# Kernel optimization log

Measured on AMD Instinct MI355X. Metric: run time of the kernel, lower is better.

Reference implementation:

```python
import jax, jax.numpy as jnp
import numpy as np

B, L_VLM, L_EXP = 4, 768, 64
L_TOT = L_VLM + L_EXP
D_VLM, D_EXP = 2048, 1024
H, DH = 8, 256
ROPE_BASE = 10000.0
SCALE = 1.0 / np.sqrt(DH).astype(np.float32)


def setup_inputs() -> dict:
    key = jax.random.key(0)
    ks = jax.random.split(key, 12)
    s = 0.02  # weight init scale
    return {
        "vlm_hidden": jax.random.normal(ks[0], (B, L_VLM, D_VLM), jnp.float32),
        "exp_hidden": jax.random.normal(ks[1], (B, L_EXP, D_EXP), jnp.float32),
        "attention_mask": jnp.zeros((B, 1, L_TOT, L_TOT), jnp.float32),  # additive mask
        "position_ids": jnp.broadcast_to(jnp.arange(L_TOT, dtype=jnp.int32)[None, :], (B, L_TOT)),
        "wq_v": jax.random.normal(ks[2], (D_VLM, H * DH), jnp.float32) * s,
        "wk_v": jax.random.normal(ks[3], (D_VLM, H * DH), jnp.float32) * s,
        "wv_v": jax.random.normal(ks[4], (D_VLM, H * DH), jnp.float32) * s,
        "wo_v": jax.random.normal(ks[5], (H * DH, D_VLM), jnp.float32) * s,
        "wq_e": jax.random.normal(ks[6], (D_EXP, H * DH), jnp.float32) * s,
        "wk_e": jax.random.normal(ks[7], (D_EXP, H * DH), jnp.float32) * s,
        "wv_e": jax.random.normal(ks[8], (D_EXP, H * DH), jnp.float32) * s,
        "wo_e": jax.random.normal(ks[9], (H * DH, D_EXP), jnp.float32) * s,
    }


def _proj(hs, w):
    # [B, L, D] @ [D, H*DH] -> [B, H, L, DH]
    b, l, _ = hs.shape
    return jnp.einsum('bld,de->ble', hs, w).reshape(b, l, H, DH).transpose(0, 2, 1, 3)


def _rope(x, cos, sin):
    # NeoX-style rotate-half (Gemma / vLLM RotaryEmbedding with rotary_dim == head_dim)
    d2 = x.shape[-1] // 2
    x1, x2 = x[..., :d2], x[..., d2:]
    return jnp.concatenate([x1 * cos - x2 * sin, x2 * cos + x1 * sin], axis=-1)


def reference(vlm_hidden, exp_hidden, attention_mask, position_ids,
              wq_v, wk_v, wv_v, wo_v, wq_e, wk_e, wv_e, wo_e):
    # 1) separate per-stream Q/K/V projections, 2) concat along sequence dim
    q = jnp.concatenate([_proj(vlm_hidden, wq_v), _proj(exp_hidden, wq_e)], axis=2)
    k = jnp.concatenate([_proj(vlm_hidden, wk_v), _proj(exp_hidden, wk_e)], axis=2)
    v = jnp.concatenate([_proj(vlm_hidden, wv_v), _proj(exp_hidden, wv_e)], axis=2)

    # 3) rotary positional embedding on the joint sequence
    inv_freq = 1.0 / (ROPE_BASE ** (jnp.arange(0, DH, 2, dtype=jnp.float32) / DH))  # [DH/2]
    freqs = position_ids.astype(jnp.float32)[:, :, None] * inv_freq                 # [B, L, DH/2]
    cos = jnp.cos(freqs)[:, None]  # [B, 1, L, DH/2]
    sin = jnp.sin(freqs)[:, None]
    q = _rope(q, cos, sin)
    k = _rope(k, cos, sin)

    # 4) masked attention over the joint sequence
    scores = jnp.einsum('bhqd,bhkd->bhqk', q, k) * SCALE + attention_mask
    probs = jax.nn.softmax(scores, axis=-1)
    out = jnp.einsum('bhqk,bhkd->bhqd', probs, v)              # [B, H, L, DH]
    out = out.transpose(0, 2, 1, 3).reshape(B, L_TOT, H * DH)  # [B, L, H*DH]

    # 5) split back and apply per-stream output projections
    vlm_out = jnp.einsum('ble,ed->bld', out[:, :L_VLM], wo_v)
    exp_out = jnp.einsum('ble,ed->bld', out[:, L_VLM:], wo_e)
    return vlm_out, exp_out
```

## Files before the change

### kernel.cpp

```cpp
#include <hip/hip_runtime.h>

typedef unsigned short u16;
using bf16x8 = __attribute__((ext_vector_type(8))) __bf16;
using f32x4  = __attribute__((ext_vector_type(4))) float;

__device__ __forceinline__ u16 f2bf(float f) {
  unsigned u = __builtin_bit_cast(unsigned, f);
  u += 0x7FFFu + ((u >> 16) & 1u);
  return (u16)(u >> 16);
}
__device__ __forceinline__ float bf2f(u16 s) {
  unsigned u = ((unsigned)s) << 16;
  return __builtin_bit_cast(float, u);
}
__device__ __forceinline__ void lds16(const void* g, void* l) {
  __builtin_amdgcn_global_load_lds(
      (const __attribute__((address_space(1))) void*)g,
      (__attribute__((address_space(3))) void*)l, 16, 0, 0);
}

#define MM(A, B, C) __builtin_amdgcn_mfma_f32_16x16x32_bf16(A, B, C, 0, 0, 0)

#define MFMA16() \
  __builtin_amdgcn_s_setprio(1); \
  acc[0][0]=MM(a0,b0,acc[0][0]); acc[0][1]=MM(a0,b1,acc[0][1]); \
  acc[0][2]=MM(a0,b2,acc[0][2]); acc[0][3]=MM(a0,b3,acc[0][3]); \
  acc[1][0]=MM(a1,b0,acc[1][0]); acc[1][1]=MM(a1,b1,acc[1][1]); \
  acc[1][2]=MM(a1,b2,acc[1][2]); acc[1][3]=MM(a1,b3,acc[1][3]); \
  acc[2][0]=MM(a2,b0,acc[2][0]); acc[2][1]=MM(a2,b1,acc[2][1]); \
  acc[2][2]=MM(a2,b2,acc[2][2]); acc[2][3]=MM(a2,b3,acc[2][3]); \
  acc[3][0]=MM(a3,b0,acc[3][0]); acc[3][1]=MM(a3,b1,acc[3][1]); \
  acc[3][2]=MM(a3,b2,acc[3][2]); acc[3][3]=MM(a3,b3,acc[3][3]); \
  __builtin_amdgcn_s_setprio(0);

__device__ __forceinline__ void gemm_rg(
    const u16* aS0, const u16* aS1, const u16* bS0,
    int NT, int t, u16* As, u16* Bs, f32x4 (&acc)[4][4])
{
  const int lane = t & 63, fr = lane & 15, q4 = lane >> 4;
  const int w = t >> 6, wm = w >> 1, wn = w & 1;
  const int sxy = (q4 ^ ((fr >> 1) & 3)) * 8;
  const int aoff = (wm * 64 + fr) * 32 + sxy;
  const int boff = (wn * 64 + fr) * 32 + sxy;

  lds16(aS0,      As + t * 8);
  lds16(aS1,      As + 4096 + t * 8);
  lds16(bS0,      Bs + t * 8);
  lds16(aS0 + 32, As + 8192 + t * 8);
  lds16(aS1 + 32, As + 8192 + 4096 + t * 8);
  lds16(bS0 + 32, Bs + 4096 + t * 8);
  asm volatile("s_waitcnt vmcnt(3)" ::: "memory");
  __builtin_amdgcn_s_barrier();

  for (int T = 0; T < NT; ++T) {
    const int q = T % 3;
    const u16* Ab = As + q * 8192;
    const u16* Bb = Bs + q * 4096;
    bf16x8 a0 = *(const bf16x8*)(Ab + aoff);
    bf16x8 a1 = *(const bf16x8*)(Ab + aoff + 512);
    bf16x8 a2 = *(const bf16x8*)(Ab + aoff + 1024);
    bf16x8 a3 = *(const bf16x8*)(Ab + aoff + 1536);
    bf16x8 b0 = *(const bf16x8*)(Bb + boff);
    bf16x8 b1 = *(const bf16x8*)(Bb + boff + 512);
    bf16x8 b2 = *(const bf16x8*)(Bb + boff + 1024);
    bf16x8 b3 = *(const bf16x8*)(Bb + boff + 1536);
    const bool s2 = (T + 2 < NT);
    if (s2) {
      const int q2 = (T + 2) % 3;
      const int k2 = (T + 2) * 32;
      lds16(aS0 + k2, As + q2 * 8192 + t * 8);
      lds16(aS1 + k2, As + q2 * 8192 + 4096 + t * 8);
      lds16(bS0 + k2, Bs + q2 * 4096 + t * 8);
    }
    __builtin_amdgcn_s_barrier();
    asm volatile("s_waitcnt lgkmcnt(0)" ::: "memory");
    __builtin_amdgcn_sched_barrier(0);
    MFMA16();
    if (s2) asm volatile("s_waitcnt vmcnt(3)" ::: "memory");
    else    asm volatile("s_waitcnt vmcnt(0)" ::: "memory");
    __builtin_amdgcn_s_barrier();
  }
}

struct PrepArgs {
  const float* tsrc[8]; u16* tdst[8]; int tK[8]; int tN[8];
  const float* csrc[2]; u16* cdst[2]; int cn4[2];
};

__global__ __launch_bounds__(256) void g_prep(PrepArgs a)
{
  __shared__ float T[32][33];
  const int z = blockIdx.z;
  if (z < 8) {
    const int Krows = a.tK[z], Ncols = a.tN[z];
    const int k0 = blockIdx.y * 32, n0 = blockIdx.x * 32;
    if (k0 >= Krows || n0 >= Ncols) return;
    const float* W = a.tsrc[z];
    u16* Wt = a.tdst[z];
    const int tx = threadIdx.x & 31, ty = threadIdx.x >> 5;
#pragma unroll
    for (int r = 0; r < 4; ++r)
      T[ty + r * 8][tx] = W[(size_t)(k0 + ty + r * 8) * Ncols + n0 + tx];
    __syncthreads();
#pragma unroll
    for (int r = 0; r < 4; ++r)
      Wt[(size_t)(n0 + ty + r * 8) * Krows + k0 + tx] = f2bf(T[tx][ty + r * 8]);
  } else {
    const int j = z - 8;
    const int n4 = a.cn4[j];
    const float* X = a.csrc[j];
    u16* Y = a.cdst[j];
    const int blk = blockIdx.y * gridDim.x + blockIdx.x;
    const int stride = gridDim.x * gridDim.y * 256;
    for (int i = blk * 256 + threadIdx.x; i < n4; i += stride) {
      float4 f = ((const float4*)X)[i];
      ushort4 u;
      u.x = f2bf(f.x); u.y = f2bf(f.y); u.z = f2bf(f.z); u.w = f2bf(f.w);
      ((ushort4*)Y)[i] = u;
    }
  }
}

__global__ __launch_bounds__(512, 4) void g_proj_qkv(
    const u16* __restrict__ Xv, const u16* __restrict__ Xe,
    const u16* __restrict__ Wv_cat, const u16* __restrict__ We_cat,
    u16* __restrict__ Qb, u16* __restrict__ Kb, u16* __restrict__ Vt)
{
  __shared__ __align__(16) u16 As[24576], Bs[12288];
  const int y = blockIdx.y;
  const u16* X; const u16* Wt; int Kdim, rows_pb, l_off, m0;
  if (y < 12) { X = Xv; Wt = Wv_cat; Kdim = 2048; rows_pb = 768; l_off = 0; m0 = y * 256; }
  else        { X = Xe; Wt = We_cat; Kdim = 1024; rows_pb = 64;  l_off = 768; m0 = 0; }
  const int t = threadIdx.x;
  const int n0 = blockIdx.x * 128;
  const int r = t >> 2;
  const int swk = ((t & 3) ^ ((t >> 3) & 3)) * 8;
  const u16* aS0 = X + (size_t)(m0 + r) * Kdim + swk;
  const u16* aS1 = X + (size_t)(m0 + r + 128) * Kdim + swk;
  const u16* bS0 = Wt + (size_t)(n0 + r) * Kdim + swk;

  f32x4 acc[4][4] = {};
  gemm_rg(aS0, aS1, bS0, Kdim >> 5, t, As, Bs, acc);

  const int lane = t & 63, fr = lane & 15, q4 = lane >> 4;
  const int w = t >> 6, wm = w >> 1, wn = w & 1;
  const int rbase = m0 + wm * 64 + q4 * 4;
  const int cbase = n0 + wn * 64 + fr;
  const int sect = n0 >> 11;

  if (sect < 2) {
    u16* Out = (sect == 0) ? Qb : Kb;
#pragma unroll
    for (int mt = 0; mt < 4; ++mt) {
#pragma unroll
      for (int rr = 0; rr < 4; ++rr) {
        int m = rbase + mt * 16 + rr;
        int b = m / rows_pb;
        int l = m - b * rows_pb + l_off;
#pragma unroll
        for (int nt = 0; nt < 4; ++nt) {
          int nloc = (cbase + nt * 16) & 2047;
          Out[(((size_t)(b * 8 + (nloc >> 8))) * 832 + l) * 256 + (nloc & 255)] =
              f2bf(acc[mt][nt][rr]);
        }
      }
    }
  } else {
#pragma unroll
    for (int mt = 0; mt < 4; ++mt) {
      int mb = rbase + mt * 16;
      int b = mb / rows_pb;
      int l = mb - b * rows_pb + l_off;
#pragma unroll
      for (int nt = 0; nt < 4; ++nt) {
        int nloc = (cbase + nt * 16) & 2047;
        ushort4 p;
        p.x = f2bf(acc[mt][nt][0]); p.y = f2bf(acc[mt][nt][1]);
        p.z = f2bf(acc[mt][nt][2]); p.w = f2bf(acc[mt][nt][3]);
        *(ushort4*)&Vt[(((size_t)(b * 8 + (nloc >> 8))) * 256 + (nloc & 255)) * 832 + l] = p;
      }
    }
  }
}

__global__ __launch_bounds__(128) void g_rope(
    u16* __restrict__ Q, u16* __restrict__ Kx, const int* __restrict__ pos)
{
  const int blk = blockIdx.x;
  const int l = blk % 832, bh = blk / 832, b = bh >> 3;
  const int i = threadIdx.x;
  const float p = (float)pos[b * 832 + l];
  const float inv = exp2f(-(float)i * 0.103810252965229910f);
  const float ang = p * inv;
  const float c = cosf(ang), s = sinf(ang);
  const size_t base = ((size_t)bh * 832 + l) * 256;

  float x1 = bf2f(Q[base + i]), x2 = bf2f(Q[base + i + 128]);
  Q[base + i]       = f2bf((x1 * c - x2 * s) * 0.0625f);
  Q[base + i + 128] = f2bf((x2 * c + x1 * s) * 0.0625f);
  x1 = bf2f(Kx[base + i]); x2 = bf2f(Kx[base + i + 128]);
  Kx[base + i]       = f2bf(x1 * c - x2 * s);
  Kx[base + i + 128] = f2bf(x2 * c + x1 * s);
}

__global__ __launch_bounds__(256) void g_flash(
    const u16* __restrict__ Qb, const u16* __restrict__ Kb,
    const u16* __restrict__ Vt, const float* __restrict__ mask,
    u16* __restrict__ AO)
{
  __shared__ __align__(16) u16 Ks[8192];
  __shared__ __align__(16) u16 Vs[8192];
  __shared__ __align__(16) u16 Ps[2048];
  const int t = threadIdx.x;
  const int lane = t & 63, w = t >> 6, quad = lane >> 4;
  const int wb = w * 512;

  const int id = blockIdx.x;
  const int x = id & 7, k = id >> 3;
  const int bh = x + 8 * (k / 13);
  const int q0 = (k % 13) * 64;
  const int b = bh >> 3, h = bh & 7;

  const u16* Ksrc = Kb + (size_t)bh * 832 * 256;
  const u16* Vsrc = Vt + (size_t)bh * 256 * 832;
  const float* Mrow = mask + (size_t)b * 832 * 832;

  bf16x8 qf[8];
#pragma unroll
  for (int kf = 0; kf < 8; ++kf)
    qf[kf] = *(const bf16x8*)(
        Qb + ((size_t)bh * 832 + q0 + w * 16 + (lane & 15)) * 256 +
        kf * 32 + quad * 8);

  float mrun[4], lrun[4];
#pragma unroll
  for (int r = 0; r < 4; ++r) { mrun[r] = -3e38f; lrun[r] = 0.f; }
  f32x4 oa[16] = {};

  for (int kt = 0; kt < 26; ++kt) {
    __syncthreads();
#pragma unroll
    for (int p = 0; p < 4; ++p) {
      int c = p * 256 + t;
      int row = c >> 5, chk = c & 31;
      lds16(Ksrc + (size_t)(kt * 32 + row) * 256 + ((chk ^ (row & 7)) * 8),
            Ks + c * 8);
    }
#pragma unroll
    for (int p = 0; p < 4; ++p) {
      int c = p * 256 + t;
      int row = c >> 3;
      int lc = (c & 7) ^ (row & 7);
      int dh = 2 * row + (lc >> 2);
      lds16(Vsrc + (size_t)dh * 832 + kt * 32 + (lc & 3) * 8, Vs + c * 8);
    }
    __syncthreads();

    f32x4 sa[2] = {};
#pragma unroll
    for (int ks = 0; ks < 8; ++ks)
#pragma unroll
      for (int nt = 0; nt < 2; ++nt) {
        int krow = nt * 16 + (lane & 15);
        bf16x8 kb = *(const bf16x8*)(
            Ks + krow * 256 + (((ks * 4 + quad) ^ (krow & 7)) * 8));
        sa[nt] = __builtin_amdgcn_mfma_f32_16x16x32_bf16(qf[ks], kb, sa[nt], 0, 0, 0);
      }

    float alpha[4];
#pragma unroll
    for (int r = 0; r < 4; ++r) {
      int prow = quad * 4 + r;
      int q = q0 + w * 16 + prow;
      const float* mrp = Mrow + (size_t)q * 832 + kt * 32 + (lane & 15);
      float v0 = sa[0][r] + mrp[0];
      float v1 = sa[1][r] + mrp[16];
      float mx = fmaxf(v0, v1);
      mx = fmaxf(mx, __shfl_xor(mx, 1));
      mx = fmaxf(mx, __shfl_xor(mx, 2));
      mx = fmaxf(mx, __shfl_xor(mx, 4));
      mx = fmaxf(mx, __shfl_xor(mx, 8));
      float mn = fmaxf(mrun[r], mx);
      float al = __expf(mrun[r] - mn);
      float p0 = __expf(v0 - mn), p1 = __expf(v1 - mn);
      float rs = p0 + p1;
      rs += __shfl_xor(rs, 1);
      rs += __shfl_xor(rs, 2);
      rs += __shfl_xor(rs, 4);
      rs += __shfl_xor(rs, 8);
      lrun[r] = lrun[r] * al + rs;
      mrun[r] = mn;
      alpha[r] = al;
      int s0 = ((lane >> 3) & 1) ^ quad;
      int s1 = (2 | ((lane >> 3) & 1)) ^ quad;
      Ps[wb + prow * 32 + s0 * 8 + (lane & 7)] = f2bf(p0);
      Ps[wb + prow * 32 + s1 * 8 + (lane & 7)] = f2bf(p1);
    }

#pragma unroll
    for (int nt = 0; nt < 16; ++nt)
#pragma unroll
      for (int r = 0; r < 4; ++r) oa[nt][r] *= alpha[r];

    int prow2 = lane & 15;
    bf16x8 pa = *(const bf16x8*)(
        Ps + wb + prow2 * 32 + ((quad ^ ((prow2 >> 2) & 3)) * 8));
#pragma unroll
    for (int nt = 0; nt < 16; ++nt) {
      int dh = nt * 16 + (lane & 15);
      int row = dh >> 1;
      int lc = ((dh & 1) << 2) | quad;
      bf16x8 vb = *(const bf16x8*)(Vs + row * 64 + ((lc ^ (row & 7)) * 8));
      oa[nt] = __builtin_amdgcn_mfma_f32_16x16x32_bf16(pa, vb, oa[nt], 0, 0, 0);
    }
  }

  float linv[4];
#pragma unroll
  for (int r = 0; r < 4; ++r) linv[r] = 1.0f / lrun[r];
#pragma unroll
  for (int r = 0; r < 4; ++r) {
    size_t l = q0 + w * 16 + quad * 4 + r;
    u16* dst = AO + ((size_t)b * 832 + l) * 2048 + h * 256 + (lane & 15);
#pragma unroll
    for (int nt = 0; nt < 16; ++nt)
      dst[nt * 16] = f2bf(oa[nt][r] * linv[r]);
  }
}

__global__ __launch_bounds__(512, 4) void g_oproj2(
    const u16* __restrict__ AO, const u16* __restrict__ Wov,
    const u16* __restrict__ Woe, float* __restrict__ out)
{
  __shared__ __align__(16) u16 As[24576], Bs[12288];
  const int y = blockIdx.y;
  const u16* Wt; float* C; int N, rows_pb, l_off, m0;
  if (y < 12) { Wt = Wov; C = out; N = 2048; rows_pb = 768; l_off = 0; m0 = y * 256; }
  else {
    if (blockIdx.x >= 8) return;
    Wt = Woe; C = out + (size_t)4 * 768 * 2048; N = 1024; rows_pb = 64; l_off = 768; m0 = 0;
  }
  const int t = threadIdx.x;
  const int n0 = blockIdx.x * 128;
  const int r = t >> 2;
  const int swk = ((t & 3) ^ ((t >> 3) & 3)) * 8;
  int mr0 = m0 + r, mr1 = m0 + r + 128;
  int ba = mr0 / rows_pb, bb = mr1 / rows_pb;
  const u16* aS0 = AO + ((size_t)ba * 832 + (mr0 - ba * rows_pb) + l_off) * 2048 + swk;
  const u16* aS1 = AO + ((size_t)bb * 832 + (mr1 - bb * rows_pb) + l_off) * 2048 + swk;
  const u16* bS0 = Wt + (size_t)(n0 + r) * 2048 + swk;

  f32x4 acc[4][4] = {};
  gemm_rg(aS0, aS1, bS0, 64, t, As, Bs, acc);

  const int lane = t & 63, fr = lane & 15, q4 = lane >> 4;
  const int w = t >> 6, wm = w >> 1, wn = w & 1;
  const int rbase = m0 + wm * 64 + q4 * 4;
  const int cbase = n0 + wn * 64 + fr;
#pragma unroll
  for (int mt = 0; mt < 4; ++mt)
#pragma unroll
    for (int rr = 0; rr < 4; ++rr) {
      size_t m = rbase + mt * 16 + rr;
#pragma unroll
      for (int nt = 0; nt < 4; ++nt)
        C[m * N + cbase + nt * 16] = acc[mt][nt][rr];
    }
}

extern "C" void kernel_launch(void* const* d_in, const int* in_sizes, int n_in,
                              void* d_out, int out_size, void* d_ws, size_t ws_size,
                              hipStream_t stream)
{
  const float* vlm_h = (const float*)d_in[0];
  const float* exp_h = (const float*)d_in[1];
  const float* mask  = (const float*)d_in[2];
  const int*   pos   = (const int*)d_in[3];
  const float* wq_v  = (const float*)d_in[4];
  const float* wk_v  = (const float*)d_in[5];
  const float* wv_v  = (const float*)d_in[6];
  const float* wo_v  = (const float*)d_in[7];
  const float* wq_e  = (const float*)d_in[8];
  const float* wk_e  = (const float*)d_in[9];
  const float* wv_e  = (const float*)d_in[10];
  const float* wo_e  = (const float*)d_in[11];
  float* out = (float*)d_out;

  u16* U = (u16*)d_ws;
  u16* Xv   = U; U += (size_t)4 * 768 * 2048;
  u16* Xe   = U; U += (size_t)4 * 64 * 1024;
  u16* Wcv  = U; U += (size_t)6144 * 2048;
  u16* Wce  = U; U += (size_t)6144 * 1024;
  u16* Wov  = U; U += (size_t)2048 * 2048;
  u16* Woe  = U; U += (size_t)1024 * 2048;
  u16* Qb   = U; U += (size_t)32 * 832 * 256;
  u16* Kb   = U; U += (size_t)32 * 832 * 256;
  u16* Vt   = U; U += (size_t)32 * 256 * 832;
  u16* AO   = U; U += (size_t)4 * 832 * 2048;

  const dim3 blk(256);

  PrepArgs pa;
  pa.tsrc[0] = wq_v; pa.tdst[0] = Wcv;                        pa.tK[0] = 2048; pa.tN[0] = 2048;
  pa.tsrc[1] = wk_v; pa.tdst[1] = Wcv + (size_t)2048 * 2048;  pa.tK[1] = 2048; pa.tN[1] = 2048;
  pa.tsrc[2] = wv_v; pa.tdst[2] = Wcv + (size_t)4096 * 2048;  pa.tK[2] = 2048; pa.tN[2] = 2048;
  pa.tsrc[3] = wo_v; pa.tdst[3] = Wov;                        pa.tK[3] = 2048; pa.tN[3] = 2048;
  pa.tsrc[4] = wq_e; pa.tdst[4] = Wce;                        pa.tK[4] = 1024; pa.tN[4] = 2048;
  pa.tsrc[5] = wk_e; pa.tdst[5] = Wce + (size_t)2048 * 1024;  pa.tK[5] = 1024; pa.tN[5] = 2048;
  pa.tsrc[6] = wv_e; pa.tdst[6] = Wce + (size_t)4096 * 1024;  pa.tK[6] = 1024; pa.tN[6] = 2048;
  pa.tsrc[7] = wo_e; pa.tdst[7] = Woe;                        pa.tK[7] = 2048; pa.tN[7] = 1024;
  pa.csrc[0] = vlm_h; pa.cdst[0] = Xv; pa.cn4[0] = 1572864;
  pa.csrc[1] = exp_h; pa.cdst[1] = Xe; pa.cn4[1] = 65536;
  g_prep<<<dim3(64, 64, 10), blk, 0, stream>>>(pa);

  g_proj_qkv<<<dim3(48, 13, 1), dim3(512), 0, stream>>>(Xv, Xe, Wcv, Wce, Qb, Kb, Vt);

  g_rope<<<dim3(32 * 832), dim3(128), 0, stream>>>(Qb, Kb, pos);

  g_flash<<<dim3(416), blk, 0, stream>>>(Qb, Kb, Vt, mask, AO);

  g_oproj2<<<dim3(16, 13, 1), dim3(512), 0, stream>>>(AO, Wov, Woe, out);
}
```

Measured before the change: 416.1 us.

## Use 4-wave GEMM blocks with 128x64 per-wave tiles in projections

The QKV and output projection GEMMs now run with 256-thread blocks instead of 512, keeping the same 256x128 block tile. Each wave computes 128x64 (8x4 MFMA tiles) instead of 64x64, so every B fragment read from LDS is reused across twice as many MFMAs. Each thread now issues six async global-to-LDS loads per stage. The intent is less LDS read traffic and fewer barrier participants per MFMA, in exchange for higher register pressure (32 accumulators) and fewer waves available to hide latency.

```diff
diff --git a/kernel.cpp b/kernel.cpp
--- a/kernel.cpp
+++ b/kernel.cpp
@@ -21,62 +21,53 @@
 
 #define MM(A, B, C) __builtin_amdgcn_mfma_f32_16x16x32_bf16(A, B, C, 0, 0, 0)
 
-#define MFMA16() \
-  __builtin_amdgcn_s_setprio(1); \
-  acc[0][0]=MM(a0,b0,acc[0][0]); acc[0][1]=MM(a0,b1,acc[0][1]); \
-  acc[0][2]=MM(a0,b2,acc[0][2]); acc[0][3]=MM(a0,b3,acc[0][3]); \
-  acc[1][0]=MM(a1,b0,acc[1][0]); acc[1][1]=MM(a1,b1,acc[1][1]); \
-  acc[1][2]=MM(a1,b2,acc[1][2]); acc[1][3]=MM(a1,b3,acc[1][3]); \
-  acc[2][0]=MM(a2,b0,acc[2][0]); acc[2][1]=MM(a2,b1,acc[2][1]); \
-  acc[2][2]=MM(a2,b2,acc[2][2]); acc[2][3]=MM(a2,b3,acc[2][3]); \
-  acc[3][0]=MM(a3,b0,acc[3][0]); acc[3][1]=MM(a3,b1,acc[3][1]); \
-  acc[3][2]=MM(a3,b2,acc[3][2]); acc[3][3]=MM(a3,b3,acc[3][3]); \
-  __builtin_amdgcn_s_setprio(0);
-
-__device__ __forceinline__ void gemm_rg(
-    const u16* aS0, const u16* aS1, const u16* bS0,
-    int NT, int t, u16* As, u16* Bs, f32x4 (&acc)[4][4])
+#define STG6(TT, QQ) \
+  lds16(aS0 + (size_t)(TT) * 32, As + (QQ) * 8192 + t * 8); \
+  lds16(aS1 + (size_t)(TT) * 32, As + (QQ) * 8192 + 2048 + t * 8); \
+  lds16(aS2 + (size_t)(TT) * 32, As + (QQ) * 8192 + 4096 + t * 8); \
+  lds16(aS3 + (size_t)(TT) * 32, As + (QQ) * 8192 + 6144 + t * 8); \
+  lds16(bS0 + (size_t)(TT) * 32, Bs + (QQ) * 4096 + t * 8); \
+  lds16(bS1 + (size_t)(TT) * 32, Bs + (QQ) * 4096 + 2048 + t * 8);
+
+__device__ __forceinline__ void gemm_w4(
+    const u16* aS0, const u16* aS1, const u16* aS2, const u16* aS3,
+    const u16* bS0, const u16* bS1,
+    int NT, int t, u16* As, u16* Bs, f32x4 (&acc)[8][4])
 {
   const int lane = t & 63, fr = lane & 15, q4 = lane >> 4;
   const int w = t >> 6, wm = w >> 1, wn = w & 1;
   const int sxy = (q4 ^ ((fr >> 1) & 3)) * 8;
-  const int aoff = (wm * 64 + fr) * 32 + sxy;
+  const int aoff = (wm * 128 + fr) * 32 + sxy;
   const int boff = (wn * 64 + fr) * 32 + sxy;
 
-  lds16(aS0,      As + t * 8);
-  lds16(aS1,      As + 4096 + t * 8);
-  lds16(bS0,      Bs + t * 8);
-  lds16(aS0 + 32, As + 8192 + t * 8);
-  lds16(aS1 + 32, As + 8192 + 4096 + t * 8);
-  lds16(bS0 + 32, Bs + 4096 + t * 8);
-  asm volatile("s_waitcnt vmcnt(3)" ::: "memory");
+  STG6(0, 0);
+  STG6(1, 1);
+  asm volatile("s_waitcnt vmcnt(6)" ::: "memory");
   __builtin_amdgcn_s_barrier();
 
   for (int T = 0; T < NT; ++T) {
     const int q = T % 3;
     const u16* Ab = As + q * 8192;
     const u16* Bb = Bs + q * 4096;
-    bf16x8 a0 = *(const bf16x8*)(Ab + aoff);
-    bf16x8 a1 = *(const bf16x8*)(Ab + aoff + 512);
-    bf16x8 a2 = *(const bf16x8*)(Ab + aoff + 1024);
-    bf16x8 a3 = *(const bf16x8*)(Ab + aoff + 1536);
-    bf16x8 b0 = *(const bf16x8*)(Bb + boff);
-    bf16x8 b1 = *(const bf16x8*)(Bb + boff + 512);
-    bf16x8 b2 = *(const bf16x8*)(Bb + boff + 1024);
-    bf16x8 b3 = *(const bf16x8*)(Bb + boff + 1536);
+    bf16x8 af[8], bfv[4];
+#pragma unroll
+    for (int mt = 0; mt < 8; ++mt)
+      af[mt] = *(const bf16x8*)(Ab + aoff + mt * 512);
+#pragma unroll
+    for (int nt = 0; nt < 4; ++nt)
+      bfv[nt] = *(const bf16x8*)(Bb + boff + nt * 512);
     const bool s2 = (T + 2 < NT);
-    if (s2) {
-      const int q2 = (T + 2) % 3;
-      const int k2 = (T + 2) * 32;
-      lds16(aS0 + k2, As + q2 * 8192 + t * 8);
-      lds16(aS1 + k2, As + q2 * 8192 + 4096 + t * 8);
-      lds16(bS0 + k2, Bs + q2 * 4096 + t * 8);
-    }
-    __builtin_amdgcn_s_barrier();
+    if (s2) { const int q2 = (T + 2) % 3; STG6(T + 2, q2); }
     asm volatile("s_waitcnt lgkmcnt(0)" ::: "memory");
     __builtin_amdgcn_sched_barrier(0);
-    MFMA16();
-    if (s2) asm volatile("s_waitcnt vmcnt(3)" ::: "memory");
+    __builtin_amdgcn_s_setprio(1);
+#pragma unroll
+    for (int mt = 0; mt < 8; ++mt)
+#pragma unroll
+      for (int nt = 0; nt < 4; ++nt)
+        acc[mt][nt] = MM(af[mt], bfv[nt], acc[mt][nt]);
+    __builtin_amdgcn_s_setprio(0);
+    if (s2) asm volatile("s_waitcnt vmcnt(6)" ::: "memory");
     else    asm volatile("s_waitcnt vmcnt(0)" ::: "memory");
     __builtin_amdgcn_s_barrier();
   }
@@ -121,7 +112,7 @@
   }
 }
 
-__global__ __launch_bounds__(512, 4) void g_proj_qkv(
+__global__ __launch_bounds__(256, 2) void g_proj_qkv(
     const u16* __restrict__ Xv, const u16* __restrict__ Xe,
     const u16* __restrict__ Wv_cat, const u16* __restrict__ We_cat,
     u16* __restrict__ Qb, u16* __restrict__ Kb, u16* __restrict__ Vt)
@@ -133,25 +124,28 @@
   else        { X = Xe; Wt = We_cat; Kdim = 1024; rows_pb = 64;  l_off = 768; m0 = 0; }
   const int t = threadIdx.x;
   const int n0 = blockIdx.x * 128;
-  const int r = t >> 2;
+  const int r0 = t >> 2;
   const int swk = ((t & 3) ^ ((t >> 3) & 3)) * 8;
-  const u16* aS0 = X + (size_t)(m0 + r) * Kdim + swk;
-  const u16* aS1 = X + (size_t)(m0 + r + 128) * Kdim + swk;
-  const u16* bS0 = Wt + (size_t)(n0 + r) * Kdim + swk;
-
-  f32x4 acc[4][4] = {};
-  gemm_rg(aS0, aS1, bS0, Kdim >> 5, t, As, Bs, acc);
+  const u16* aS0 = X + (size_t)(m0 + r0) * Kdim + swk;
+  const u16* aS1 = X + (size_t)(m0 + r0 + 64) * Kdim + swk;
+  const u16* aS2 = X + (size_t)(m0 + r0 + 128) * Kdim + swk;
+  const u16* aS3 = X + (size_t)(m0 + r0 + 192) * Kdim + swk;
+  const u16* bS0 = Wt + (size_t)(n0 + r0) * Kdim + swk;
+  const u16* bS1 = Wt + (size_t)(n0 + r0 + 64) * Kdim + swk;
+
+  f32x4 acc[8][4] = {};
+  gemm_w4(aS0, aS1, aS2, aS3, bS0, bS1, Kdim >> 5, t, As, Bs, acc);
 
   const int lane = t & 63, fr = lane & 15, q4 = lane >> 4;
   const int w = t >> 6, wm = w >> 1, wn = w & 1;
-  const int rbase = m0 + wm * 64 + q4 * 4;
+  const int rbase = m0 + wm * 128 + q4 * 4;
   const int cbase = n0 + wn * 64 + fr;
   const int sect = n0 >> 11;
 
   if (sect < 2) {
     u16* Out = (sect == 0) ? Qb : Kb;
 #pragma unroll
-    for (int mt = 0; mt < 4; ++mt) {
+    for (int mt = 0; mt < 8; ++mt) {
 #pragma unroll
       for (int rr = 0; rr < 4; ++rr) {
         int m = rbase + mt * 16 + rr;
@@ -167,7 +161,7 @@
     }
   } else {
 #pragma unroll
-    for (int mt = 0; mt < 4; ++mt) {
+    for (int mt = 0; mt < 8; ++mt) {
       int mb = rbase + mt * 16;
       int b = mb / rows_pb;
       int l = mb - b * rows_pb + l_off;
@@ -328,7 +322,7 @@
   }
 }
 
-__global__ __launch_bounds__(512, 4) void g_oproj2(
+__global__ __launch_bounds__(256, 2) void g_oproj2(
     const u16* __restrict__ AO, const u16* __restrict__ Wov,
     const u16* __restrict__ Woe, float* __restrict__ out)
 {
@@ -342,23 +336,27 @@
   }
   const int t = threadIdx.x;
   const int n0 = blockIdx.x * 128;
-  const int r = t >> 2;
+  const int r0 = t >> 2;
   const int swk = ((t & 3) ^ ((t >> 3) & 3)) * 8;
-  int mr0 = m0 + r, mr1 = m0 + r + 128;
-  int ba = mr0 / rows_pb, bb = mr1 / rows_pb;
-  const u16* aS0 = AO + ((size_t)ba * 832 + (mr0 - ba * rows_pb) + l_off) * 2048 + swk;
-  const u16* aS1 = AO + ((size_t)bb * 832 + (mr1 - bb * rows_pb) + l_off) * 2048 + swk;
-  const u16* bS0 = Wt + (size_t)(n0 + r) * 2048 + swk;
-
-  f32x4 acc[4][4] = {};
-  gemm_rg(aS0, aS1, bS0, 64, t, As, Bs, acc);
+  const u16* aSp[4];
+#pragma unroll
+  for (int i = 0; i < 4; ++i) {
+    int mr = m0 + i * 64 + r0;
+    int ba = mr / rows_pb;
+    aSp[i] = AO + ((size_t)ba * 832 + (mr - ba * rows_pb) + l_off) * 2048 + swk;
+  }
+  const u16* bS0 = Wt + (size_t)(n0 + r0) * 2048 + swk;
+  const u16* bS1 = Wt + (size_t)(n0 + r0 + 64) * 2048 + swk;
+
+  f32x4 acc[8][4] = {};
+  gemm_w4(aSp[0], aSp[1], aSp[2], aSp[3], bS0, bS1, 64, t, As, Bs, acc);
 
   const int lane = t & 63, fr = lane & 15, q4 = lane >> 4;
   const int w = t >> 6, wm = w >> 1, wn = w & 1;
-  const int rbase = m0 + wm * 64 + q4 * 4;
+  const int rbase = m0 + wm * 128 + q4 * 4;
   const int cbase = n0 + wn * 64 + fr;
 #pragma unroll
-  for (int mt = 0; mt < 4; ++mt)
+  for (int mt = 0; mt < 8; ++mt)
 #pragma unroll
     for (int rr = 0; rr < 4; ++rr) {
       size_t m = rbase + mt * 16 + rr;
@@ -413,11 +411,11 @@
   pa.csrc[1] = exp_h; pa.cdst[1] = Xe; pa.cn4[1] = 65536;
   g_prep<<<dim3(64, 64, 10), blk, 0, stream>>>(pa);
 
-  g_proj_qkv<<<dim3(48, 13, 1), dim3(512), 0, stream>>>(Xv, Xe, Wcv, Wce, Qb, Kb, Vt);
+  g_proj_qkv<<<dim3(48, 13, 1), blk, 0, stream>>>(Xv, Xe, Wcv, Wce, Qb, Kb, Vt);
 
   g_rope<<<dim3(32 * 832), dim3(128), 0, stream>>>(Qb, Kb, pos);
 
   g_flash<<<dim3(416), blk, 0, stream>>>(Qb, Kb, Vt, mask, AO);
 
-  g_oproj2<<<dim3(16, 13, 1), dim3(512), 0, stream>>>(AO, Wov, Woe, out);
-}
+  g_oproj2<<<dim3(16, 13, 1), blk, 0, stream>>>(AO, Wov, Woe, out);
+}
```

After: 415.4 us. Within noise of the previous version (-0.2%).
